# Kernel optimization log

Measured on AMD Instinct MI355X. Metric: run time of the kernel, lower is better.

Reference implementation:

```python
import jax, jax.numpy as jnp
import numpy as np

B, HH, WW, E = 8, 128, 128, 192
NH = 8
D1 = (3 * E) // NH * NH  # 576
HD = D1 // NH            # 72
RPE = 512
LAYERS = 3
EPS = 1e-8


def srms(x):
    # SimpleRMSNorm: x / (||x||_2 / sqrt(d) + eps), no learned params
    d = x.shape[-1]
    norm = jnp.linalg.norm(x, axis=-1, keepdims=True)
    return x / (norm * (d ** -0.5) + EPS)


def rpe_net(idx, pos_w, pos_b, lw, lb, out_w, out_b):
    # idx: (L, 1) float positions -> (NH, L, HD) Toeplitz coefficients
    h = idx @ pos_w.T + pos_b  # (L, RPE)
    for i in range(LAYERS):   # residual=False
        h = jax.nn.relu(srms(h)) @ lw[i].T + lb[i]
    h = jax.nn.relu(srms(h)) @ out_w.T + out_b  # (L, NH*HD)
    return h.reshape(idx.shape[0], NH, HD).transpose(1, 0, 2)


def tno(v, axis, pos_w, pos_b, lw, lb, out_w, out_b):
    # v: (b, h, H, W, d); Toeplitz mixing along `axis` (-3 or -2), non-causal,
    # par_type=1, no decay, act_type='none', normalize=False.
    n = v.shape[axis]
    z = jnp.zeros((1,), jnp.float32)
    p = jnp.arange(1, n, dtype=jnp.float32)
    # coefficient layout for length-2n circular conv: a0, a1..a(n-1), a0, a-(n-1)..a-1
    idx = jnp.concatenate([z, p, z, -p[::-1]]).reshape(-1, 1)  # (2n, 1)
    a = rpe_net(idx, pos_w, pos_b, lw, lb, out_w, out_b)       # (NH, 2n, HD)
    ak = a[:, None, :, :] if axis == -2 else a[:, :, None, :]
    y = jnp.fft.rfft(v, 2 * n, axis=axis)
    af = jnp.fft.rfft(ak, 2 * n, axis=axis)
    out = jnp.fft.irfft(af * y, 2 * n, axis=axis)
    return out[..., :n, :] if axis == -2 else out[..., :n, :, :]


def setup_inputs() -> dict:
    key = jax.random.key(0)
    ks = jax.random.split(key, 19)
    s = 0.02
    rn = lambda k, shape, sc=s: jax.random.normal(k, shape, dtype=jnp.float32) * sc
    inp = {
        'x': jax.random.normal(ks[0], (B, HH, WW, E), dtype=jnp.float32),
        'u_w': rn(ks[1], (D1, E)), 'u_b': rn(ks[2], (D1,)),
        'v_w': rn(ks[3], (D1, E)), 'v_b': rn(ks[4], (D1,)),
        'o_w': rn(ks[5], (E, D1)), 'o_b': rn(ks[6], (E,)),
    }
    for i, name in enumerate(['rpe1', 'rpe2']):
        off = 7 + i * 6
        inp[name + '_pos_w'] = rn(ks[off], (RPE, 1), 0.5)
        inp[name + '_pos_b'] = rn(ks[off + 1], (RPE,), 0.5)
        inp[name + '_lw'] = rn(ks[off + 2], (LAYERS, RPE, RPE))
        inp[name + '_lb'] = rn(ks[off + 3], (LAYERS, RPE))
        inp[name + '_out_w'] = rn(ks[off + 4], (NH * HD, RPE))
        inp[name + '_out_b'] = rn(ks[off + 5], (NH * HD,))
    inp['H'] = HH
    inp['W'] = WW
    return inp


def reference(x, u_w, u_b, v_w, v_b, o_w, o_b,
              rpe1_pos_w, rpe1_pos_b, rpe1_lw, rpe1_lb, rpe1_out_w, rpe1_out_b,
              rpe2_pos_w, rpe2_pos_b, rpe2_lw, rpe2_lb, rpe2_out_w, rpe2_out_b,
              H, W):
    shortcut = x
    xn = srms(x)                              # pre_norm (SimpleRMSNorm)
    u = jax.nn.silu(xn @ u_w.T + u_b)         # (B,H,W,D1)
    v = jax.nn.silu(xn @ v_w.T + v_b)
    b = v.shape[0]
    v = v.reshape(b, H, W, NH, HD).transpose(0, 3, 1, 2, 4)  # b h H W d
    out = (tno(v, -3, rpe2_pos_w, rpe2_pos_b, rpe2_lw, rpe2_lb, rpe2_out_w, rpe2_out_b)
           + tno(v, -2, rpe1_pos_w, rpe1_pos_b, rpe1_lw, rpe1_lb, rpe1_out_w, rpe1_out_b))
    out = out.transpose(0, 2, 3, 1, 4).reshape(b, H, W, NH * HD)  # b H W (h d)
    out = u * out
    return out @ o_w.T + o_b + shortcut
```

## Files before the change

kernel.cpp:

```cpp
#include <hip/hip_runtime.h>
#include <hip/hip_bf16.h>

typedef __hip_bfloat16 bf16;
typedef __attribute__((ext_vector_type(4))) float f32x4;
typedef __attribute__((ext_vector_type(8))) __bf16 bf16x8;
typedef __attribute__((ext_vector_type(4))) __bf16 bf16x4;

constexpr int NB  = 8;
constexpr int NHH = 128;
constexpr int NWW = 128;
constexpr int NE  = 192;
constexpr int ND  = 576;
constexpr int NR  = 512;
constexpr int NL  = 256;
constexpr int NP  = NB * NHH * NWW;
constexpr int NPC = NHH * NWW;

__device__ __forceinline__ void gload16(const void* g, void* l) {
    __builtin_amdgcn_global_load_lds(
        (const __attribute__((address_space(1))) unsigned int*)g,
        (__attribute__((address_space(3))) unsigned int*)l, 16, 0, 0);
}

__global__ void k_rpe_pos(const float* __restrict__ pw1, const float* __restrict__ pb1,
                          const float* __restrict__ pw2, const float* __restrict__ pb2,
                          float* __restrict__ h)
{
    int net = blockIdx.x >> 8;
    int l   = blockIdx.x & 255;
    const float* pw = net ? pw2 : pw1;
    const float* pb = net ? pb2 : pb1;
    float idxv;
    if (l == 0 || l == 128) idxv = 0.f;
    else if (l < 128)       idxv = (float)l;
    else                    idxv = (float)(l - 256);
    float* hr = h + ((size_t)net * NL + l) * NR;
    for (int r = threadIdx.x; r < NR; r += 256)
        hr[r] = idxv * pw[r] + pb[r];
}

__global__ __launch_bounds__(256) void k_wt(
    const float* __restrict__ lw1, const float* __restrict__ ow1,
    const float* __restrict__ lw2, const float* __restrict__ ow2,
    float* __restrict__ wt)
{
    __shared__ float tile[32][33];
    int m = blockIdx.z, net = m >> 2, sub = m & 3;
    int J = (sub == 3) ? 576 : 512;
    const float* src = (sub == 3) ? (net ? ow2 : ow1)
                                  : (net ? lw2 : lw1) + (size_t)sub * 262144;
    float* dst = wt + (size_t)net * 1081344 + ((sub == 3) ? 786432 : sub * 262144);
    int r0 = blockIdx.x * 32, j0 = blockIdx.y * 32;
    if (j0 >= J) return;
    int tx = threadIdx.x, ty = threadIdx.y;
    #pragma unroll
    for (int d = 0; d < 4; ++d) {
        int j = j0 + ty + d * 8;
        tile[ty + d * 8][tx] = (j < J) ? src[(size_t)j * 512 + r0 + tx] : 0.f;
    }
    __syncthreads();
    #pragma unroll
    for (int d = 0; d < 4; ++d) {
        int r = r0 + ty + d * 8;
        int j = j0 + tx;
        if (j < J) dst[(size_t)r * J + j] = tile[tx][ty + d * 8];
    }
}

__global__ __launch_bounds__(256) void k_rpe_layer(
    const float* __restrict__ hin,
    const float* __restrict__ Wt1, const float* __restrict__ b1,
    const float* __restrict__ Wt2, const float* __restrict__ b2,
    float* __restrict__ out1, float* __restrict__ out2, int outdim)
{
    __shared__ float g[2][NR];
    __shared__ float red[256];
    int net = blockIdx.x >> 7;
    int l0  = (blockIdx.x & 127) * 2;
    const float* hr = hin + ((size_t)net * NL + l0) * NR;
    int tid = threadIdx.x;
    int row = tid >> 7, ix = tid & 127;
    const float* hh = hr + (size_t)row * NR;
    float a0 = hh[ix], a1 = hh[ix + 128], a2 = hh[ix + 256], a3 = hh[ix + 384];
    red[tid] = a0 * a0 + a1 * a1 + a2 * a2 + a3 * a3;
    __syncthreads();
    for (int off = 64; off; off >>= 1) {
        if (ix < off) red[tid] += red[tid + off];
        __syncthreads();
    }
    float sc = 1.f / (sqrtf(red[row << 7]) * 0.044194173824159216f + 1e-8f);
    g[row][ix]       = fmaxf(a0 * sc, 0.f);
    g[row][ix + 128] = fmaxf(a1 * sc, 0.f);
    g[row][ix + 256] = fmaxf(a2 * sc, 0.f);
    g[row][ix + 384] = fmaxf(a3 * sc, 0.f);
    __syncthreads();
    const float* Wt = net ? Wt2 : Wt1;
    const float* bb = net ? b2 : b1;
    float* o0 = (net ? out2 : out1) + (size_t)l0 * outdim;
    int half = outdim >> 1;
    for (int jj = tid; jj < half; jj += 256) {
        float ax0 = 0.f, ay0 = 0.f, ax1 = 0.f, ay1 = 0.f;
        const float* wp = Wt + 2 * jj;
        #pragma unroll 8
        for (int r = 0; r < NR; ++r) {
            float2 w = *(const float2*)(wp + (size_t)r * outdim);
            float g0 = g[0][r], g1 = g[1][r];
            ax0 = fmaf(g0, w.x, ax0); ay0 = fmaf(g0, w.y, ay0);
            ax1 = fmaf(g1, w.x, ax1); ay1 = fmaf(g1, w.y, ay1);
        }
        float bx = bb[2 * jj], by = bb[2 * jj + 1];
        o0[2 * jj]              = ax0 + bx;  o0[2 * jj + 1]          = ay0 + by;
        o0[outdim + 2 * jj]     = ax1 + bx;  o0[outdim + 2 * jj + 1] = ay1 + by;
    }
}

__global__ __launch_bounds__(256) void k_toep(
    const float* __restrict__ A1, const float* __restrict__ A2, bf16* __restrict__ T)
{
    __shared__ float Als[256][17];
    int cb = blockIdx.x, rq = blockIdx.y, net = blockIdx.z;
    const float* A = net ? A2 : A1;
    int tid = threadIdx.x;
    #pragma unroll
    for (int i = 0; i < 16; ++i) {
        int el = i * 256 + tid;
        int k = el >> 4, cl = el & 15;
        Als[k][cl] = A[(size_t)k * ND + cb * 16 + cl];
    }
    __syncthreads();
    int cl = tid >> 4, sg = tid & 15;
    __bf16* Tb = (__bf16*)T + (((size_t)net * ND + cb * 16 + cl) * 128) * 128;
    for (int rr = 0; rr < 32; ++rr) {
        int r = rq * 32 + rr;
        bf16x8 o;
        #pragma unroll
        for (int j = 0; j < 8; ++j) {
            int s = sg * 8 + j;
            o[j] = (__bf16)Als[(r - s) & 255][cl];
        }
        *(bf16x8*)(Tb + (size_t)r * 128 + sg * 8) = o;
    }
}

__global__ void k_prep(const float* __restrict__ x, bf16* __restrict__ xbn)
{
    __shared__ __bf16 wbuf[4][208];
    int w = threadIdx.x >> 6, lane = threadIdx.x & 63;
    int p = blockIdx.x * 4 + w;
    const float* xp = x + (size_t)p * NE;
    float v0 = xp[lane], v1 = xp[lane + 64], v2 = xp[lane + 128];
    float ss = v0 * v0 + v1 * v1 + v2 * v2;
    for (int off = 32; off; off >>= 1) ss += __shfl_xor(ss, off, 64);
    float sc = __builtin_amdgcn_rcpf(sqrtf(ss) * 0.07216878364870323f + 1e-8f);
    wbuf[w][lane]       = (__bf16)(v0 * sc);
    wbuf[w][lane + 64]  = (__bf16)(v1 * sc);
    wbuf[w][lane + 128] = (__bf16)(v2 * sc);
    __syncthreads();
    if (lane < 24) {
        bf16x8 o = *(bf16x8*)&wbuf[w][lane * 8];
        int t = (lane & 24) | ((lane & 7) ^ (p & 7));
        *(bf16x8*)((__bf16*)xbn + (size_t)p * NE + t * 8) = o;
    }
}

__global__ void k_wconv(const float* __restrict__ uw, const float* __restrict__ vw,
                        const float* __restrict__ ow,
                        bf16* __restrict__ wb, bf16* __restrict__ owb)
{
    int gid = blockIdx.x * 256 + threadIdx.x;
    if (gid < 27648) {
        int row = gid / 24, bb = gid - row * 24;
        const float* src = ((row < ND) ? uw + (size_t)row * NE
                                       : vw + (size_t)(row - ND) * NE) + bb * 8;
        float4 f0 = ((const float4*)src)[0], f1 = ((const float4*)src)[1];
        bf16x8 o;
        o[0] = (__bf16)f0.x; o[1] = (__bf16)f0.y; o[2] = (__bf16)f0.z; o[3] = (__bf16)f0.w;
        o[4] = (__bf16)f1.x; o[5] = (__bf16)f1.y; o[6] = (__bf16)f1.z; o[7] = (__bf16)f1.w;
        int t = (bb & 24) | ((bb & 7) ^ (row & 7));
        *(bf16x8*)((__bf16*)wb + (size_t)row * NE + t * 8) = o;
    } else if (gid < 27648 + 13824) {
        int g = gid - 27648;
        const float* src = ow + (size_t)g * 8;
        float4 f0 = ((const float4*)src)[0], f1 = ((const float4*)src)[1];
        bf16x8 o;
        o[0] = (__bf16)f0.x; o[1] = (__bf16)f0.y; o[2] = (__bf16)f0.z; o[3] = (__bf16)f0.w;
        o[4] = (__bf16)f1.x; o[5] = (__bf16)f1.y; o[6] = (__bf16)f1.z; o[7] = (__bf16)f1.w;
        *(bf16x8*)((__bf16*)owb + (size_t)g * 8) = o;
    }
}

__global__ __launch_bounds__(256) void k_uv(
    const bf16* __restrict__ xbn, const bf16* __restrict__ wb,
    const float* __restrict__ ub, const float* __restrict__ vb,
    bf16* __restrict__ u_t, bf16* __restrict__ v_t)
{
    __shared__ __align__(16) char smem[32768];
    __bf16 (*sA)[64] = (__bf16(*)[64])smem;
    __bf16 (*sB)[64] = (__bf16(*)[64])(smem + 16384);
    __bf16* ldst = (__bf16*)smem;
    int tid = threadIdx.x;
    int wv = tid >> 6, lane = tid & 63;
    int b = blockIdx.x;
    int chunk = b & 7;
    int s = b >> 3;
    int by = s / 9;
    int ntile = s - by * 9;
    int nbase = ntile * 128;
    int wr = wv >> 1, wc = wv & 1;
    int lrow = lane >> 3, lcol = lane & 7;
    size_t gbase = (size_t)chunk * NPC + by * 128;
    f32x4 acc[4][4] = {};
    for (int kk = 0; kk < 3; ++kk) {
        #pragma unroll
        for (int i = 0; i < 4; ++i) {
            int row = wv * 32 + i * 8;
            gload16((const char*)(xbn + (gbase + row + lrow) * NE + kk * 64) + lcol * 16,
                    &sA[row][0]);
            gload16((const char*)(wb + (size_t)(nbase + row + lrow) * NE + kk * 64) + lcol * 16,
                    &sB[row][0]);
        }
        asm volatile("s_waitcnt vmcnt(0)" ::: "memory");
        __syncthreads();
        int q = lane >> 4, fr = lane & 15;
        #pragma unroll
        for (int k2 = 0; k2 < 2; ++k2) {
            bf16x8 af[4], bw[4];
            #pragma unroll
            for (int m = 0; m < 4; ++m) {
                int frm = wr * 64 + m * 16 + fr;
                af[m] = *(const bf16x8*)&sA[frm][(((k2 << 2) | q) ^ (frm & 7)) * 8];
            }
            #pragma unroll
            for (int n = 0; n < 4; ++n) {
                int fn = wc * 64 + n * 16 + fr;
                bw[n] = *(const bf16x8*)&sB[fn][(((k2 << 2) | q) ^ (fn & 7)) * 8];
            }
            #pragma unroll
            for (int m = 0; m < 4; ++m)
                #pragma unroll
                for (int n = 0; n < 4; ++n)
                    acc[m][n] = __builtin_amdgcn_mfma_f32_16x16x32_bf16(af[m], bw[n], acc[m][n], 0, 0, 0);
        }
        __syncthreads();
    }
    int fr = lane & 15, fq = lane >> 4;
    size_t pgl = gbase + (tid & 15) * 8;
    #pragma unroll
    for (int h = 0; h < 2; ++h) {
        if (wc == h) {
            #pragma unroll
            for (int m = 0; m < 4; ++m) {
                #pragma unroll
                for (int n = 0; n < 4; ++n) {
                    int row = n * 16 + fr;
                    int jn_g = nbase + h * 64 + row;
                    float bias = (jn_g < ND) ? ub[jn_g] : vb[jn_g - ND];
                    bf16x4 val;
                    #pragma unroll
                    for (int j = 0; j < 4; ++j) {
                        float z = acc[m][n][j] + bias;
                        float sgl = z * __builtin_amdgcn_rcpf(1.f + __expf(-z));
                        val[j] = (__bf16)sgl;
                    }
                    *(bf16x4*)&ldst[row * 132 + wr * 64 + m * 16 + fq * 4] = val;
                }
            }
        }
        __syncthreads();
        #pragma unroll
        for (int pass = 0; pass < 4; ++pass) {
            int row = (tid >> 4) + pass * 16;
            int jn_g = nbase + h * 64 + row;
            int colb = (tid & 15) * 8;
            bf16x4 a = *(bf16x4*)&ldst[row * 132 + colb];
            bf16x4 bb = *(bf16x4*)&ldst[row * 132 + colb + 4];
            bf16x8 o;
            #pragma unroll
            for (int i = 0; i < 4; ++i) { o[i] = a[i]; o[i + 4] = bb[i]; }
            __bf16* dst = (jn_g < ND) ? (__bf16*)u_t + (size_t)jn_g * NP + pgl
                                      : (__bf16*)v_t + (size_t)(jn_g - ND) * NP + pgl;
            *(bf16x8*)dst = o;
        }
        __syncthreads();
    }
}

__global__ __launch_bounds__(256) void k_conv(
    bf16* __restrict__ v_t, const bf16* __restrict__ T, const bf16* __restrict__ u_t)
{
    __shared__ __bf16 Vp[128][132];
    int tid = threadIdx.x;
    int b = blockIdx.x;
    int c = (b & 7) * 72 + ((b >> 3) >> 3);
    int chunk = (b >> 3) & 7;
    size_t pbase = (size_t)c * NP + (size_t)chunk * NPC;
    const __bf16* vsrc = (const __bf16*)v_t + pbase;
    #pragma unroll
    for (int it = 0; it < 8; ++it) {
        int y = (tid >> 4) + 16 * it;
        int x0 = (tid & 15) * 8;
        bf16x8 rd = *(const bf16x8*)(vsrc + (size_t)y * 128 + x0);
        bf16x4 lo, hi;
        #pragma unroll
        for (int i = 0; i < 4; ++i) { lo[i] = rd[i]; hi[i] = rd[i + 4]; }
        *(bf16x4*)&Vp[y][x0]     = lo;
        *(bf16x4*)&Vp[y][x0 + 4] = hi;
    }
    __syncthreads();
    int wv = tid >> 6, lane = tid & 63;
    int wr = wv >> 1, wc = wv & 1;
    int fr = lane & 15, q = lane >> 4;
    const __bf16* T1 = (const __bf16*)T + (size_t)c * 16384;
    const __bf16* T2 = (const __bf16*)T + (size_t)(ND + c) * 16384;
    f32x4 acc[4][4] = {};
    #pragma unroll
    for (int k = 0; k < 4; ++k) {
        bf16x8 af[4], bw[4];
        #pragma unroll
        for (int m = 0; m < 4; ++m) {
            int row = wr * 64 + m * 16 + fr;
            bf16x4 a = *(const bf16x4*)&Vp[row][k * 32 + q * 8];
            bf16x4 bb = *(const bf16x4*)&Vp[row][k * 32 + q * 8 + 4];
            #pragma unroll
            for (int i = 0; i < 4; ++i) { af[m][i] = a[i]; af[m][i + 4] = bb[i]; }
        }
        #pragma unroll
        for (int n = 0; n < 4; ++n)
            bw[n] = *(const bf16x8*)(T1 + (size_t)(wc * 64 + n * 16 + fr) * 128 + k * 32 + q * 8);
        #pragma unroll
        for (int m = 0; m < 4; ++m)
            #pragma unroll
            for (int n = 0; n < 4; ++n)
                acc[m][n] = __builtin_amdgcn_mfma_f32_16x16x32_bf16(af[m], bw[n], acc[m][n], 0, 0, 0);
    }
    #pragma unroll
    for (int k = 0; k < 4; ++k) {
        bf16x8 a2[4], b2[4];
        #pragma unroll
        for (int m = 0; m < 4; ++m)
            a2[m] = *(const bf16x8*)(T2 + (size_t)(wr * 64 + m * 16 + fr) * 128 + k * 32 + q * 8);
        #pragma unroll
        for (int n = 0; n < 4; ++n) {
            int xc = wc * 64 + n * 16 + fr;
            #pragma unroll
            for (int j = 0; j < 8; ++j)
                b2[n][j] = Vp[k * 32 + q * 8 + j][xc];
        }
        #pragma unroll
        for (int m = 0; m < 4; ++m)
            #pragma unroll
            for (int n = 0; n < 4; ++n)
                acc[m][n] = __builtin_amdgcn_mfma_f32_16x16x32_bf16(a2[m], b2[n], acc[m][n], 0, 0, 0);
    }
    __syncthreads();
    #pragma unroll
    for (int m = 0; m < 4; ++m) {
        #pragma unroll
        for (int n = 0; n < 4; ++n) {
            int xc = wc * 64 + n * 16 + fr;
            #pragma unroll
            for (int j = 0; j < 4; ++j) {
                int y = wr * 64 + m * 16 + q * 4 + j;
                Vp[y][xc] = (__bf16)acc[m][n][j];
            }
        }
    }
    __syncthreads();
    const __bf16* usrc = (const __bf16*)u_t + pbase;
    __bf16* vdst = (__bf16*)v_t + pbase;
    #pragma unroll
    for (int it = 0; it < 8; ++it) {
        int y = (tid >> 4) + 16 * it;
        int x0 = (tid & 15) * 8;
        bf16x8 uu = *(const bf16x8*)(usrc + (size_t)y * 128 + x0);
        bf16x4 lo = *(const bf16x4*)&Vp[y][x0];
        bf16x4 hi = *(const bf16x4*)&Vp[y][x0 + 4];
        bf16x8 o;
        #pragma unroll
        for (int i = 0; i < 4; ++i) {
            o[i]     = (__bf16)((float)uu[i]     * (float)lo[i]);
            o[i + 4] = (__bf16)((float)uu[i + 4] * (float)hi[i]);
        }
        *(bf16x8*)(vdst + (size_t)y * 128 + x0) = o;
    }
}

__global__ __launch_bounds__(256) void k_out(
    const bf16* __restrict__ g_t, const bf16* __restrict__ owb,
    const float* __restrict__ ob, const float* __restrict__ x, float* __restrict__ out)
{
    __shared__ __bf16 gs[64][132];
    int tid = threadIdx.x;
    int pt = blockIdx.x;
    int wv = tid >> 6, lane = tid & 63;
    int wr = wv >> 1, wc = wv & 1;
    int fr = lane & 15, q = lane >> 4;
    f32x4 acc[4][6] = {};
    for (int kk = 0; kk < 9; ++kk) {
        #pragma unroll
        for (int i = 0; i < 4; ++i) {
            int cl = (tid >> 4) + 16 * i;
            int pg = (tid & 15) * 8;
            bf16x8 rd = *(const bf16x8*)((const __bf16*)g_t + (size_t)(kk * 64 + cl) * NP
                                         + (size_t)pt * 128 + pg);
            bf16x4 lo, hi;
            #pragma unroll
            for (int ii = 0; ii < 4; ++ii) { lo[ii] = rd[ii]; hi[ii] = rd[ii + 4]; }
            *(bf16x4*)&gs[cl][pg]     = lo;
            *(bf16x4*)&gs[cl][pg + 4] = hi;
        }
        __syncthreads();
        #pragma unroll
        for (int ks = 0; ks < 2; ++ks) {
            bf16x8 af[4], bw[6];
            #pragma unroll
            for (int m = 0; m < 4; ++m) {
                int prow = wr * 64 + m * 16 + fr;
                #pragma unroll
                for (int j = 0; j < 8; ++j)
                    af[m][j] = gs[ks * 32 + q * 8 + j][prow];
            }
            #pragma unroll
            for (int n = 0; n < 6; ++n) {
                int e = wc * 96 + n * 16 + fr;
                bw[n] = *(const bf16x8*)((const __bf16*)owb + (size_t)e * ND + kk * 64 + ks * 32 + q * 8);
            }
            #pragma unroll
            for (int m = 0; m < 4; ++m)
                #pragma unroll
                for (int n = 0; n < 6; ++n)
                    acc[m][n] = __builtin_amdgcn_mfma_f32_16x16x32_bf16(af[m], bw[n], acc[m][n], 0, 0, 0);
        }
        __syncthreads();
    }
    #pragma unroll
    for (int m = 0; m < 4; ++m) {
        #pragma unroll
        for (int n = 0; n < 6; ++n) {
            int e = wc * 96 + n * 16 + fr;
            float bias = ob[e];
            #pragma unroll
            for (int j = 0; j < 4; ++j) {
                size_t p = (size_t)pt * 128 + wr * 64 + m * 16 + q * 4 + j;
                out[p * NE + e] = acc[m][n][j] + bias + x[p * NE + e];
            }
        }
    }
}

extern "C" void kernel_launch(void* const* d_in, const int* in_sizes, int n_in,
                              void* d_out, int out_size, void* d_ws, size_t ws_size,
                              hipStream_t stream)
{
    const float* x    = (const float*)d_in[0];
    const float* u_w  = (const float*)d_in[1];
    const float* u_b  = (const float*)d_in[2];
    const float* v_w  = (const float*)d_in[3];
    const float* v_b  = (const float*)d_in[4];
    const float* o_w  = (const float*)d_in[5];
    const float* o_b  = (const float*)d_in[6];
    const float* r1_pw = (const float*)d_in[7];
    const float* r1_pb = (const float*)d_in[8];
    const float* r1_lw = (const float*)d_in[9];
    const float* r1_lb = (const float*)d_in[10];
    const float* r1_ow = (const float*)d_in[11];
    const float* r1_ob = (const float*)d_in[12];
    const float* r2_pw = (const float*)d_in[13];
    const float* r2_pb = (const float*)d_in[14];
    const float* r2_lw = (const float*)d_in[15];
    const float* r2_lb = (const float*)d_in[16];
    const float* r2_ow = (const float*)d_in[17];
    const float* r2_ob = (const float*)d_in[18];
    float* out = (float*)d_out;

    float* A1  = (float*)d_ws;
    float* A2  = A1 + (size_t)NL * ND;
    bf16* wb   = (bf16*)(A2 + (size_t)NL * ND);
    bf16* owb  = wb + (size_t)2 * ND * NE;
    bf16* u_t  = owb + (size_t)NE * ND;
    bf16* v_t  = u_t + (size_t)ND * NP;
    bf16* xbn  = v_t + (size_t)ND * NP;
    float* h0 = (float*)(xbn + (size_t)NP * NE);
    float* h1 = h0 + (size_t)2 * NL * NR;
    float* wt = h1 + (size_t)2 * NL * NR;
    bf16* T   = (bf16*)h0;

    k_rpe_pos<<<dim3(512), dim3(256), 0, stream>>>(r1_pw, r1_pb, r2_pw, r2_pb, h0);
    k_wt<<<dim3(16, 18, 8), dim3(32, 8), 0, stream>>>(r1_lw, r1_ow, r2_lw, r2_ow, wt);
    {
        const float* src[3] = { h0, h1, h0 };
        float* dst[3]       = { h1, h0, h1 };
        for (int i = 0; i < 3; ++i) {
            k_rpe_layer<<<dim3(256), dim3(256), 0, stream>>>(
                src[i], wt + (size_t)i * 262144, r1_lb + (size_t)i * NR,
                        wt + 1081344 + (size_t)i * 262144, r2_lb + (size_t)i * NR,
                dst[i], dst[i] + (size_t)NL * NR, NR);
        }
        k_rpe_layer<<<dim3(256), dim3(256), 0, stream>>>(
            h1, wt + 786432, r1_ob, wt + 1081344 + 786432, r2_ob, A1, A2, ND);
    }
    k_toep<<<dim3(36, 4, 2), dim3(256), 0, stream>>>(A1, A2, T);
    k_wconv<<<dim3(162), dim3(256), 0, stream>>>(u_w, v_w, o_w, wb, owb);
    k_prep<<<dim3(32768), dim3(256), 0, stream>>>(x, xbn);

    k_uv<<<dim3(9216), dim3(256), 0, stream>>>(xbn, wb, u_b, v_b, u_t, v_t);
    k_conv<<<dim3(4608), dim3(256), 0, stream>>>(v_t, T, u_t);
    k_out<<<dim3(1024), dim3(256), 0, stream>>>(v_t, owb, o_b, x, out);
}
```

Measured before the change: 581.5 us.

## Merge prep kernels into two launches and XOR-swizzle LDS tiles in conv/out

Combines the RPE position and weight-transpose kernels into one launch, and the Toeplitz build, input normalization and weight conversion into another, cutting launch count. Applies an XOR swizzle to the shared-memory tiles in the conv and output kernels so that column-wise fragment reads hit fewer LDS bank conflicts. Adds an occupancy hint of 4 blocks per SM to k_uv, which may force register spills. The merged kernels branch on block index, so every block reserves the largest shared-memory footprint of the fused paths.

```diff
diff --git a/kernel.cpp b/kernel.cpp
--- a/kernel.cpp
+++ b/kernel.cpp
@@ -22,48 +22,51 @@
         (__attribute__((address_space(3))) unsigned int*)l, 16, 0, 0);
 }
 
-__global__ void k_rpe_pos(const float* __restrict__ pw1, const float* __restrict__ pb1,
-                          const float* __restrict__ pw2, const float* __restrict__ pb2,
-                          float* __restrict__ h)
-{
-    int net = blockIdx.x >> 8;
-    int l   = blockIdx.x & 255;
-    const float* pw = net ? pw2 : pw1;
-    const float* pb = net ? pb2 : pb1;
-    float idxv;
-    if (l == 0 || l == 128) idxv = 0.f;
-    else if (l < 128)       idxv = (float)l;
-    else                    idxv = (float)(l - 256);
-    float* hr = h + ((size_t)net * NL + l) * NR;
-    for (int r = threadIdx.x; r < NR; r += 256)
-        hr[r] = idxv * pw[r] + pb[r];
-}
-
-__global__ __launch_bounds__(256) void k_wt(
+__global__ __launch_bounds__(256) void k_pre1(
+    const float* __restrict__ pw1, const float* __restrict__ pb1,
+    const float* __restrict__ pw2, const float* __restrict__ pb2,
     const float* __restrict__ lw1, const float* __restrict__ ow1,
     const float* __restrict__ lw2, const float* __restrict__ ow2,
-    float* __restrict__ wt)
+    float* __restrict__ h, float* __restrict__ wt)
 {
     __shared__ float tile[32][33];
-    int m = blockIdx.z, net = m >> 2, sub = m & 3;
-    int J = (sub == 3) ? 576 : 512;
-    const float* src = (sub == 3) ? (net ? ow2 : ow1)
-                                  : (net ? lw2 : lw1) + (size_t)sub * 262144;
-    float* dst = wt + (size_t)net * 1081344 + ((sub == 3) ? 786432 : sub * 262144);
-    int r0 = blockIdx.x * 32, j0 = blockIdx.y * 32;
-    if (j0 >= J) return;
-    int tx = threadIdx.x, ty = threadIdx.y;
-    #pragma unroll
-    for (int d = 0; d < 4; ++d) {
-        int j = j0 + ty + d * 8;
-        tile[ty + d * 8][tx] = (j < J) ? src[(size_t)j * 512 + r0 + tx] : 0.f;
-    }
-    __syncthreads();
-    #pragma unroll
-    for (int d = 0; d < 4; ++d) {
-        int r = r0 + ty + d * 8;
-        int j = j0 + tx;
-        if (j < J) dst[(size_t)r * J + j] = tile[tx][ty + d * 8];
+    int b = blockIdx.x;
+    if (b < 512) {
+        int net = b >> 8, l = b & 255;
+        const float* pw = net ? pw2 : pw1;
+        const float* pb = net ? pb2 : pb1;
+        float idxv;
+        if (l == 0 || l == 128) idxv = 0.f;
+        else if (l < 128)       idxv = (float)l;
+        else                    idxv = (float)(l - 256);
+        float* hr = h + ((size_t)net * NL + l) * NR;
+        for (int r = threadIdx.x; r < NR; r += 256)
+            hr[r] = idxv * pw[r] + pb[r];
+    } else {
+        int idx = b - 512;
+        int m = idx / 288;
+        int rem = idx - m * 288;
+        int jb = rem >> 4, rb = rem & 15;
+        int net = m >> 2, sub = m & 3;
+        int J = (sub == 3) ? 576 : 512;
+        const float* src = (sub == 3) ? (net ? ow2 : ow1)
+                                      : (net ? lw2 : lw1) + (size_t)sub * 262144;
+        float* dst = wt + (size_t)net * 1081344 + ((sub == 3) ? 786432 : sub * 262144);
+        int r0 = rb * 32, j0 = jb * 32;
+        if (j0 >= J) return;
+        int tx = threadIdx.x & 31, ty = threadIdx.x >> 5;
+        #pragma unroll
+        for (int d = 0; d < 4; ++d) {
+            int j = j0 + ty + d * 8;
+            tile[ty + d * 8][tx] = (j < J) ? src[(size_t)j * 512 + r0 + tx] : 0.f;
+        }
+        __syncthreads();
+        #pragma unroll
+        for (int d = 0; d < 4; ++d) {
+            int r = r0 + ty + d * 8;
+            int j = j0 + tx;
+            if (j < J) dst[(size_t)r * J + j] = tile[tx][ty + d * 8];
+        }
     }
 }
 
@@ -114,82 +117,80 @@
     }
 }
 
-__global__ __launch_bounds__(256) void k_toep(
-    const float* __restrict__ A1, const float* __restrict__ A2, bf16* __restrict__ T)
-{
-    __shared__ float Als[256][17];
-    int cb = blockIdx.x, rq = blockIdx.y, net = blockIdx.z;
-    const float* A = net ? A2 : A1;
+__global__ __launch_bounds__(256) void k_pre2(
+    const float* __restrict__ x, bf16* __restrict__ xbn,
+    const float* __restrict__ A1, const float* __restrict__ A2, bf16* __restrict__ T,
+    const float* __restrict__ uw, const float* __restrict__ vw,
+    const float* __restrict__ ow, bf16* __restrict__ wb, bf16* __restrict__ owb)
+{
+    __shared__ __align__(16) char sm[17408];
+    int b = blockIdx.x;
     int tid = threadIdx.x;
-    #pragma unroll
-    for (int i = 0; i < 16; ++i) {
-        int el = i * 256 + tid;
-        int k = el >> 4, cl = el & 15;
-        Als[k][cl] = A[(size_t)k * ND + cb * 16 + cl];
-    }
-    __syncthreads();
-    int cl = tid >> 4, sg = tid & 15;
-    __bf16* Tb = (__bf16*)T + (((size_t)net * ND + cb * 16 + cl) * 128) * 128;
-    for (int rr = 0; rr < 32; ++rr) {
-        int r = rq * 32 + rr;
-        bf16x8 o;
-        #pragma unroll
-        for (int j = 0; j < 8; ++j) {
-            int s = sg * 8 + j;
-            o[j] = (__bf16)Als[(r - s) & 255][cl];
-        }
-        *(bf16x8*)(Tb + (size_t)r * 128 + sg * 8) = o;
-    }
-}
-
-__global__ void k_prep(const float* __restrict__ x, bf16* __restrict__ xbn)
-{
-    __shared__ __bf16 wbuf[4][208];
-    int w = threadIdx.x >> 6, lane = threadIdx.x & 63;
-    int p = blockIdx.x * 4 + w;
-    const float* xp = x + (size_t)p * NE;
-    float v0 = xp[lane], v1 = xp[lane + 64], v2 = xp[lane + 128];
-    float ss = v0 * v0 + v1 * v1 + v2 * v2;
-    for (int off = 32; off; off >>= 1) ss += __shfl_xor(ss, off, 64);
-    float sc = __builtin_amdgcn_rcpf(sqrtf(ss) * 0.07216878364870323f + 1e-8f);
-    wbuf[w][lane]       = (__bf16)(v0 * sc);
-    wbuf[w][lane + 64]  = (__bf16)(v1 * sc);
-    wbuf[w][lane + 128] = (__bf16)(v2 * sc);
-    __syncthreads();
-    if (lane < 24) {
-        bf16x8 o = *(bf16x8*)&wbuf[w][lane * 8];
-        int t = (lane & 24) | ((lane & 7) ^ (p & 7));
-        *(bf16x8*)((__bf16*)xbn + (size_t)p * NE + t * 8) = o;
-    }
-}
-
-__global__ void k_wconv(const float* __restrict__ uw, const float* __restrict__ vw,
-                        const float* __restrict__ ow,
-                        bf16* __restrict__ wb, bf16* __restrict__ owb)
-{
-    int gid = blockIdx.x * 256 + threadIdx.x;
-    if (gid < 27648) {
-        int row = gid / 24, bb = gid - row * 24;
-        const float* src = ((row < ND) ? uw + (size_t)row * NE
-                                       : vw + (size_t)(row - ND) * NE) + bb * 8;
-        float4 f0 = ((const float4*)src)[0], f1 = ((const float4*)src)[1];
-        bf16x8 o;
-        o[0] = (__bf16)f0.x; o[1] = (__bf16)f0.y; o[2] = (__bf16)f0.z; o[3] = (__bf16)f0.w;
-        o[4] = (__bf16)f1.x; o[5] = (__bf16)f1.y; o[6] = (__bf16)f1.z; o[7] = (__bf16)f1.w;
-        int t = (bb & 24) | ((bb & 7) ^ (row & 7));
-        *(bf16x8*)((__bf16*)wb + (size_t)row * NE + t * 8) = o;
-    } else if (gid < 27648 + 13824) {
-        int g = gid - 27648;
-        const float* src = ow + (size_t)g * 8;
-        float4 f0 = ((const float4*)src)[0], f1 = ((const float4*)src)[1];
-        bf16x8 o;
-        o[0] = (__bf16)f0.x; o[1] = (__bf16)f0.y; o[2] = (__bf16)f0.z; o[3] = (__bf16)f0.w;
-        o[4] = (__bf16)f1.x; o[5] = (__bf16)f1.y; o[6] = (__bf16)f1.z; o[7] = (__bf16)f1.w;
-        *(bf16x8*)((__bf16*)owb + (size_t)g * 8) = o;
-    }
-}
-
-__global__ __launch_bounds__(256) void k_uv(
+    if (b < 32768) {
+        __bf16 (*wbuf)[208] = (__bf16(*)[208])sm;
+        int w = tid >> 6, lane = tid & 63;
+        int p = b * 4 + w;
+        const float* xp = x + (size_t)p * NE;
+        float v0 = xp[lane], v1 = xp[lane + 64], v2 = xp[lane + 128];
+        float ss = v0 * v0 + v1 * v1 + v2 * v2;
+        for (int off = 32; off; off >>= 1) ss += __shfl_xor(ss, off, 64);
+        float sc = __builtin_amdgcn_rcpf(sqrtf(ss) * 0.07216878364870323f + 1e-8f);
+        wbuf[w][lane]       = (__bf16)(v0 * sc);
+        wbuf[w][lane + 64]  = (__bf16)(v1 * sc);
+        wbuf[w][lane + 128] = (__bf16)(v2 * sc);
+        __syncthreads();
+        if (lane < 24) {
+            bf16x8 o = *(bf16x8*)&wbuf[w][lane * 8];
+            int t = (lane & 24) | ((lane & 7) ^ (p & 7));
+            *(bf16x8*)((__bf16*)xbn + (size_t)p * NE + t * 8) = o;
+        }
+    } else if (b < 32768 + 288) {
+        float (*Als)[17] = (float(*)[17])sm;
+        int i = b - 32768;
+        int cb = i % 36, rq = (i / 36) & 3, net = i / 144;
+        const float* A = net ? A2 : A1;
+        #pragma unroll
+        for (int it = 0; it < 16; ++it) {
+            int el = it * 256 + tid;
+            int k = el >> 4, cl = el & 15;
+            Als[k][cl] = A[(size_t)k * ND + cb * 16 + cl];
+        }
+        __syncthreads();
+        int cl = tid >> 4, sg = tid & 15;
+        __bf16* Tb = (__bf16*)T + (((size_t)net * ND + cb * 16 + cl) * 128) * 128;
+        for (int rr = 0; rr < 32; ++rr) {
+            int r = rq * 32 + rr;
+            bf16x8 o;
+            #pragma unroll
+            for (int j = 0; j < 8; ++j)
+                o[j] = (__bf16)Als[(r - sg * 8 - j) & 255][cl];
+            *(bf16x8*)(Tb + (size_t)r * 128 + sg * 8) = o;
+        }
+    } else {
+        int gid = (b - 33056) * 256 + tid;
+        if (gid < 27648) {
+            int row = gid / 24, bb = gid - row * 24;
+            const float* src = ((row < ND) ? uw + (size_t)row * NE
+                                           : vw + (size_t)(row - ND) * NE) + bb * 8;
+            float4 f0 = ((const float4*)src)[0], f1 = ((const float4*)src)[1];
+            bf16x8 o;
+            o[0] = (__bf16)f0.x; o[1] = (__bf16)f0.y; o[2] = (__bf16)f0.z; o[3] = (__bf16)f0.w;
+            o[4] = (__bf16)f1.x; o[5] = (__bf16)f1.y; o[6] = (__bf16)f1.z; o[7] = (__bf16)f1.w;
+            int t = (bb & 24) | ((bb & 7) ^ (row & 7));
+            *(bf16x8*)((__bf16*)wb + (size_t)row * NE + t * 8) = o;
+        } else if (gid < 27648 + 13824) {
+            int g = gid - 27648;
+            const float* src = ow + (size_t)g * 8;
+            float4 f0 = ((const float4*)src)[0], f1 = ((const float4*)src)[1];
+            bf16x8 o;
+            o[0] = (__bf16)f0.x; o[1] = (__bf16)f0.y; o[2] = (__bf16)f0.z; o[3] = (__bf16)f0.w;
+            o[4] = (__bf16)f1.x; o[5] = (__bf16)f1.y; o[6] = (__bf16)f1.z; o[7] = (__bf16)f1.w;
+            *(bf16x8*)((__bf16*)owb + (size_t)g * 8) = o;
+        }
+    }
+}
+
+__global__ __launch_bounds__(256, 4) void k_uv(
     const bf16* __restrict__ xbn, const bf16* __restrict__ wb,
     const float* __restrict__ ub, const float* __restrict__ vb,
     bf16* __restrict__ u_t, bf16* __restrict__ v_t)
@@ -298,13 +299,14 @@
     #pragma unroll
     for (int it = 0; it < 8; ++it) {
         int y = (tid >> 4) + 16 * it;
-        int x0 = (tid & 15) * 8;
-        bf16x8 rd = *(const bf16x8*)(vsrc + (size_t)y * 128 + x0);
+        int xblk = tid & 15;
+        bf16x8 rd = *(const bf16x8*)(vsrc + (size_t)y * 128 + xblk * 8);
+        int col = ((xblk ^ ((y >> 3) & 7))) * 8;
         bf16x4 lo, hi;
         #pragma unroll
         for (int i = 0; i < 4; ++i) { lo[i] = rd[i]; hi[i] = rd[i + 4]; }
-        *(bf16x4*)&Vp[y][x0]     = lo;
-        *(bf16x4*)&Vp[y][x0 + 4] = hi;
+        *(bf16x4*)&Vp[y][col]     = lo;
+        *(bf16x4*)&Vp[y][col + 4] = hi;
     }
     __syncthreads();
     int wv = tid >> 6, lane = tid & 63;
@@ -319,8 +321,9 @@
         #pragma unroll
         for (int m = 0; m < 4; ++m) {
             int row = wr * 64 + m * 16 + fr;
-            bf16x4 a = *(const bf16x4*)&Vp[row][k * 32 + q * 8];
-            bf16x4 bb = *(const bf16x4*)&Vp[row][k * 32 + q * 8 + 4];
+            int col = (((k * 4 + q) ^ ((row >> 3) & 7))) * 8;
+            bf16x4 a = *(const bf16x4*)&Vp[row][col];
+            bf16x4 bb = *(const bf16x4*)&Vp[row][col + 4];
             #pragma unroll
             for (int i = 0; i < 4; ++i) { af[m][i] = a[i]; af[m][i + 4] = bb[i]; }
         }
@@ -343,8 +346,11 @@
         for (int n = 0; n < 4; ++n) {
             int xc = wc * 64 + n * 16 + fr;
             #pragma unroll
-            for (int j = 0; j < 8; ++j)
-                b2[n][j] = Vp[k * 32 + q * 8 + j][xc];
+            for (int j = 0; j < 8; ++j) {
+                int row = k * 32 + q * 8 + j;
+                int col = (((xc >> 3) ^ ((row >> 3) & 7))) * 8 + (xc & 7);
+                b2[n][j] = Vp[row][col];
+            }
         }
         #pragma unroll
         for (int m = 0; m < 4; ++m)
@@ -361,7 +367,8 @@
             #pragma unroll
             for (int j = 0; j < 4; ++j) {
                 int y = wr * 64 + m * 16 + q * 4 + j;
-                Vp[y][xc] = (__bf16)acc[m][n][j];
+                int col = (((xc >> 3) ^ ((y >> 3) & 7))) * 8 + (xc & 7);
+                Vp[y][col] = (__bf16)acc[m][n][j];
             }
         }
     }
@@ -371,17 +378,18 @@
     #pragma unroll
     for (int it = 0; it < 8; ++it) {
         int y = (tid >> 4) + 16 * it;
-        int x0 = (tid & 15) * 8;
-        bf16x8 uu = *(const bf16x8*)(usrc + (size_t)y * 128 + x0);
-        bf16x4 lo = *(const bf16x4*)&Vp[y][x0];
-        bf16x4 hi = *(const bf16x4*)&Vp[y][x0 + 4];
+        int xblk = tid & 15;
+        int col = ((xblk ^ ((y >> 3) & 7))) * 8;
+        bf16x8 uu = *(const bf16x8*)(usrc + (size_t)y * 128 + xblk * 8);
+        bf16x4 lo = *(const bf16x4*)&Vp[y][col];
+        bf16x4 hi = *(const bf16x4*)&Vp[y][col + 4];
         bf16x8 o;
         #pragma unroll
         for (int i = 0; i < 4; ++i) {
             o[i]     = (__bf16)((float)uu[i]     * (float)lo[i]);
             o[i + 4] = (__bf16)((float)uu[i + 4] * (float)hi[i]);
         }
-        *(bf16x8*)(vdst + (size_t)y * 128 + x0) = o;
+        *(bf16x8*)(vdst + (size_t)y * 128 + xblk * 8) = o;
     }
 }
 
@@ -400,14 +408,15 @@
         #pragma unroll
         for (int i = 0; i < 4; ++i) {
             int cl = (tid >> 4) + 16 * i;
-            int pg = (tid & 15) * 8;
+            int pblk = tid & 15;
             bf16x8 rd = *(const bf16x8*)((const __bf16*)g_t + (size_t)(kk * 64 + cl) * NP
-                                         + (size_t)pt * 128 + pg);
+                                         + (size_t)pt * 128 + pblk * 8);
+            int col = ((pblk ^ ((cl >> 3) & 7))) * 8;
             bf16x4 lo, hi;
             #pragma unroll
             for (int ii = 0; ii < 4; ++ii) { lo[ii] = rd[ii]; hi[ii] = rd[ii + 4]; }
-            *(bf16x4*)&gs[cl][pg]     = lo;
-            *(bf16x4*)&gs[cl][pg + 4] = hi;
+            *(bf16x4*)&gs[cl][col]     = lo;
+            *(bf16x4*)&gs[cl][col + 4] = hi;
         }
         __syncthreads();
         #pragma unroll
@@ -417,8 +426,11 @@
             for (int m = 0; m < 4; ++m) {
                 int prow = wr * 64 + m * 16 + fr;
                 #pragma unroll
-                for (int j = 0; j < 8; ++j)
-                    af[m][j] = gs[ks * 32 + q * 8 + j][prow];
+                for (int j = 0; j < 8; ++j) {
+                    int row = ks * 32 + q * 8 + j;
+                    int col = (((prow >> 3) ^ ((row >> 3) & 7))) * 8 + (prow & 7);
+                    af[m][j] = gs[row][col];
+                }
             }
             #pragma unroll
             for (int n = 0; n < 6; ++n) {
@@ -485,8 +497,8 @@
     float* wt = h1 + (size_t)2 * NL * NR;
     bf16* T   = (bf16*)h0;
 
-    k_rpe_pos<<<dim3(512), dim3(256), 0, stream>>>(r1_pw, r1_pb, r2_pw, r2_pb, h0);
-    k_wt<<<dim3(16, 18, 8), dim3(32, 8), 0, stream>>>(r1_lw, r1_ow, r2_lw, r2_ow, wt);
+    k_pre1<<<dim3(2816), dim3(256), 0, stream>>>(
+        r1_pw, r1_pb, r2_pw, r2_pb, r1_lw, r1_ow, r2_lw, r2_ow, h0, wt);
     {
         const float* src[3] = { h0, h1, h0 };
         float* dst[3]       = { h1, h0, h1 };
@@ -499,9 +511,8 @@
         k_rpe_layer<<<dim3(256), dim3(256), 0, stream>>>(
             h1, wt + 786432, r1_ob, wt + 1081344 + 786432, r2_ob, A1, A2, ND);
     }
-    k_toep<<<dim3(36, 4, 2), dim3(256), 0, stream>>>(A1, A2, T);
-    k_wconv<<<dim3(162), dim3(256), 0, stream>>>(u_w, v_w, o_w, wb, owb);
-    k_prep<<<dim3(32768), dim3(256), 0, stream>>>(x, xbn);
+    k_pre2<<<dim3(33272), dim3(256), 0, stream>>>(
+        x, xbn, A1, A2, T, u_w, v_w, o_w, wb, owb);
 
     k_uv<<<dim3(9216), dim3(256), 0, stream>>>(xbn, wb, u_b, v_b, u_t, v_t);
     k_conv<<<dim3(4608), dim3(256), 0, stream>>>(v_t, T, u_t);
```

Result: no change. 579.9 us (-0.3%).
